# Kernel tuning notes

Hardware: AMD Instinct MI355X
Metric: run time of the kernel (lower is better)

## Reference

```python
import jax, jax.numpy as jnp
import numpy as np

SEQ = 784  # 28*28, hard-coded by the module's view() calls
RES_CH = 32
DILATIONS = [1, 2, 4, 8, 16] * 2  # layer_size=5, stack_size=2


def setup_inputs() -> dict:
    key = jax.random.key(0)
    ks = jax.random.split(key, 9)
    B = 2048
    s = 0.1
    return {
        "x": jax.random.normal(ks[0], (B, 1, 28, 28), dtype=jnp.float32),
        "w_causal": jax.random.normal(ks[1], (RES_CH, 1, 2), dtype=jnp.float32) * s,
        "b_causal": jax.random.normal(ks[2], (RES_CH,), dtype=jnp.float32) * s,
        "w_dil": jax.random.normal(ks[3], (10, 2 * RES_CH, RES_CH, 2), dtype=jnp.float32) * s,
        "b_dil": jax.random.normal(ks[4], (10, 2 * RES_CH), dtype=jnp.float32) * s,
        "w_res": jax.random.normal(ks[5], (10, RES_CH, RES_CH), dtype=jnp.float32) * s,
        "b_res": jax.random.normal(ks[6], (10, RES_CH), dtype=jnp.float32) * s,
        "w_out": jax.random.normal(ks[7], (1, RES_CH), dtype=jnp.float32) * s,
        "b_out": jax.random.normal(ks[8], (1,), dtype=jnp.float32) * s,
    }


def _shift_right(h, d):
    # causal left-pad by d, keep original length: out[:, :, t] = h[:, :, t - d]
    return jnp.pad(h, ((0, 0), (0, 0), (d, 0)))[:, :, :SEQ]


def reference(x, w_causal, b_causal, w_dil, b_dil, w_res, b_res, w_out, b_out):
    B = x.shape[0]
    h = x.reshape(B, 1, SEQ)
    # Mask-A causal conv (kernel=2, dilation=1, pad [2,0], drop last):
    # y[t] = W[:,:,0] @ x[t-2] + W[:,:,1] @ x[t-1]  (strictly causal)
    y = (
        jnp.einsum("oi,bit->bot", w_causal[:, :, 0], _shift_right(h, 2))
        + jnp.einsum("oi,bit->bot", w_causal[:, :, 1], _shift_right(h, 1))
        + b_causal[None, :, None]
    )
    h = y
    # Residual stack: Mask-B dilated conv -> gated tanh*sigmoid -> 1x1 conv -> residual add
    for i, d in enumerate(DILATIONS):
        z = (
            jnp.einsum("oi,bit->bot", w_dil[i, :, :, 0], _shift_right(h, d))
            + jnp.einsum("oi,bit->bot", w_dil[i, :, :, 1], h)
            + b_dil[i][None, :, None]
        )  # [B, 2*RES_CH, SEQ]
        o1, o2 = z[:, :RES_CH], z[:, RES_CH:]
        gated = jnp.tanh(o1) * jax.nn.sigmoid(o2)
        h = h + jnp.einsum("oi,bit->bot", w_res[i], gated) + b_res[i][None, :, None]
    logits = jnp.einsum("oi,bit->bot", w_out, h) + b_out[None, :, None]
    return logits.reshape(B, 1, 28, 28)
```

## Files before the change

### kernel.cpp

```cpp
#include <hip/hip_runtime.h>

#define SEQ   784
#define PADT  16
#define NROW  (PADT + 784)
#define NWAVE 8
#define BLK   (NWAVE * 64)
#define LDS_BYTES (NROW * 32 * 2)

#define WS_WR_OFF 81920
#define WS_BD_OFF 102400
#define SC_TANH (-2.885390082f)
#define SC_SIGM (-1.442695041f)

typedef __attribute__((ext_vector_type(8))) short  short8;
typedef __attribute__((ext_vector_type(4))) float  float4v;
typedef __attribute__((ext_vector_type(2))) unsigned int uint2v;

#if __has_builtin(__builtin_amdgcn_cvt_pk_bf16_f32)
typedef __attribute__((ext_vector_type(2))) __bf16 bf16x2;
__device__ __forceinline__ unsigned int pk_rne(float lo, float hi) {
    union { bf16x2 v; unsigned int u; } r;
    r.v = __builtin_amdgcn_cvt_pk_bf16_f32(lo, hi);
    return r.u;
}
#else
__device__ __forceinline__ unsigned int pk_rne(float lo, float hi) {
    unsigned int a = __float_as_uint(lo);
    unsigned int b = __float_as_uint(hi);
    a += 0x7fffu + ((a >> 16) & 1u);
    b += 0x7fffu + ((b >> 16) & 1u);
    return __builtin_amdgcn_perm(b, a, 0x07060302);
}
#endif
__device__ __forceinline__ unsigned short f2bf(float f) {
    unsigned int a = __float_as_uint(f);
    a += 0x7fffu + ((a >> 16) & 1u);
    return (unsigned short)(a >> 16);
}
__device__ __forceinline__ void gate_pair(float a1, float b1, float a2, float b2,
                                          float& g1, float& g2) {
    a1 = __builtin_amdgcn_fmed3f(a1, -30.f, 30.f);
    b1 = __builtin_amdgcn_fmed3f(b1, -30.f, 30.f);
    a2 = __builtin_amdgcn_fmed3f(a2, -30.f, 30.f);
    b2 = __builtin_amdgcn_fmed3f(b2, -30.f, 30.f);
    float ta1 = __builtin_amdgcn_exp2f(a1), tb1 = __builtin_amdgcn_exp2f(b1);
    float ta2 = __builtin_amdgcn_exp2f(a2), tb2 = __builtin_amdgcn_exp2f(b2);
    float p1 = (1.0f + ta1) * (1.0f + tb1);
    float p2 = (1.0f + ta2) * (1.0f + tb2);
    float r  = __builtin_amdgcn_rcpf(p1 * p2);
    g1 = (1.0f - ta1) * p2 * r;
    g2 = (1.0f - ta2) * p1 * r;
}

__global__ void __launch_bounds__(64) prep_kernel(
    const float* __restrict__ w_dil, const float* __restrict__ b_dil,
    const float* __restrict__ w_res, unsigned char* __restrict__ ws)
{
    const int L    = blockIdx.x;
    const int lane = threadIdx.x;
    const int m    = lane & 15;
    const int q    = lane >> 4;
    short8* WSA = (short8*)ws;
    short8* WSR = (short8*)(ws + WS_WR_OFF);
    float*  WSB = (float*)(ws + WS_BD_OFF);

    #pragma unroll
    for (int rt = 0; rt < 4; ++rt) {
        const float sc = (rt < 2) ? SC_TANH : SC_SIGM;
        const float4* wp = (const float4*)(w_dil + (((L * 64 + rt * 16 + m) * 32) + q * 8) * 2);
        float4 c0 = wp[0], c1 = wp[1], c2 = wp[2], c3 = wp[3];
        union { unsigned int i[4]; short8 v; } u0, u1;
        u0.i[0] = pk_rne(sc * c0.x, sc * c0.z); u0.i[1] = pk_rne(sc * c1.x, sc * c1.z);
        u0.i[2] = pk_rne(sc * c2.x, sc * c2.z); u0.i[3] = pk_rne(sc * c3.x, sc * c3.z);
        u1.i[0] = pk_rne(sc * c0.y, sc * c0.w); u1.i[1] = pk_rne(sc * c1.y, sc * c1.w);
        u1.i[2] = pk_rne(sc * c2.y, sc * c2.w); u1.i[3] = pk_rne(sc * c3.y, sc * c3.w);
        WSA[((L * 4 + rt) * 2 + 0) * 64 + lane] = u0.v;
        WSA[((L * 4 + rt) * 2 + 1) * 64 + lane] = u1.v;
    }
    #pragma unroll
    for (int rt = 0; rt < 2; ++rt) {
        const float4* wp = (const float4*)(w_res + (L * 32 + rt * 16 + m) * 32 + q * 8);
        float4 d0 = wp[0], d1 = wp[1];
        union { unsigned int i[4]; short8 v; } u;
        u.i[0] = pk_rne(d0.x, d0.y); u.i[1] = pk_rne(d0.z, d0.w);
        u.i[2] = pk_rne(d1.x, d1.y); u.i[3] = pk_rne(d1.z, d1.w);
        WSR[(L * 2 + rt) * 64 + lane] = u.v;
    }
    WSB[L * 64 + lane] = b_dil[L * 64 + lane] * ((lane < 32) ? SC_TANH : SC_SIGM);
}

__global__ void __launch_bounds__(BLK, 4) wavenet_kernel(
    const float* __restrict__ x,
    const float* __restrict__ w_causal,
    const float* __restrict__ b_causal,
    const float* __restrict__ b_res,
    const float* __restrict__ w_out,
    const float* __restrict__ b_out,
    const unsigned char* __restrict__ ws,
    float* __restrict__ out)
{
    extern __shared__ unsigned short lds[];
    unsigned short* H = lds;

    const int tid = threadIdx.x;
    const int b   = blockIdx.x;

    {
        unsigned int* p = (unsigned int*)H;
        if (tid < PADT * 16) p[tid] = 0u;
    }

    {
        int o = tid & 31;
        const int gsh = (o >> 3) << 3;
        const int oo  = o & 7;
        float wc0 = w_causal[o * 2 + 0];
        float wc1 = w_causal[o * 2 + 1];
        float bc  = b_causal[o];
        const float* xb = x + b * SEQ;
        for (int idx = tid; idx < SEQ * 32; idx += BLK) {
            int t = idx >> 5;
            float v = bc;
            if (t >= 2) v += wc0 * xb[t - 2];
            if (t >= 1) v += wc1 * xb[t - 1];
            int r = PADT + t;
            int sw = ((r >> 1) & 3) << 3;
            H[r * 32 + (gsh ^ sw) + oo] = f2bf(v);
        }
    }
    __syncthreads();

    const int lane = tid & 63;
    const int wave = tid >> 6;
    const int m    = lane & 15;
    const int q    = lane >> 4;
    const int adr1 = (32 * (q & 1) + m) * 4;
    const int adr2 = adr1 + 64;
    const int hi   = q >> 1;
    const int rowu0 = PADT + wave * 16 + m;
    const int su    = (rowu0 >> 1) & 3;
    const int offBu = ((q ^ su) << 3);
    const int offH1 = (((q >> 1) ^ su) << 3) + 4 * (q & 1);
    const int offH2 = ((((q >> 1) + 2) ^ su) << 3) + 4 * (q & 1);

    short8 I0, I1;
    #pragma unroll
    for (int j = 0; j < 8; ++j) {
        I0[j] = (q * 8 + j == m)      ? (short)0x3F80 : (short)0;
        I1[j] = (q * 8 + j == m + 16) ? (short)0x3F80 : (short)0;
    }

    const short8* WSA = (const short8*)ws;
    const short8* WSR = (const short8*)(ws + WS_WR_OFF);
    const float*  WSB = (const float*)(ws + WS_BD_OFF);

    const int dil[10] = {1, 2, 4, 8, 16, 1, 2, 4, 8, 16};

    for (int L = 0; L < 10; ++L) {
        const int d = dil[L];

        short8 WA[4][2], WR[2];
        #pragma unroll
        for (int rt = 0; rt < 4; ++rt) {
            WA[rt][0] = WSA[((L * 4 + rt) * 2 + 0) * 64 + lane];
            WA[rt][1] = WSA[((L * 4 + rt) * 2 + 1) * 64 + lane];
        }
        WR[0] = WSR[(L * 2 + 0) * 64 + lane];
        WR[1] = WSR[(L * 2 + 1) * 64 + lane];
        float4v BDv[4], BRv[2];
        #pragma unroll
        for (int rt = 0; rt < 4; ++rt)
            BDv[rt] = *(const float4v*)(WSB + L * 64 + rt * 16 + q * 4);
        #pragma unroll
        for (int rt = 0; rt < 2; ++rt) {
            const float* bp = b_res + L * 32 + rt * 16 + q * 4;
            BRv[rt] = (float4v){bp[0], bp[1], bp[2], bp[3]};
        }
        const int rs0   = rowu0 - d;
        const int offBs = ((q ^ ((rs0 >> 1) & 3)) << 3);

        auto do_tile = [&](int s, uint2v& n0, uint2v& n1) {
            const int rbase  = (rowu0 + s * (NWAVE * 16)) * 32;
            const int rbases = (rs0   + s * (NWAVE * 16)) * 32;
            const short8 Bs = *(const short8*)(H + rbases + offBs);
            const short8 Bu = *(const short8*)(H + rbase + offBu);

            float4v r0 = BRv[0], r1 = BRv[1];
            r0 = __builtin_amdgcn_mfma_f32_16x16x32_bf16(I0, Bu, r0, 0, 0, 0);
            r1 = __builtin_amdgcn_mfma_f32_16x16x32_bf16(I1, Bu, r1, 0, 0, 0);

            float4v a0 = BDv[0], a1 = BDv[1], a2 = BDv[2], a3 = BDv[3];
            a0 = __builtin_amdgcn_mfma_f32_16x16x32_bf16(WA[0][0], Bs, a0, 0, 0, 0);
            a0 = __builtin_amdgcn_mfma_f32_16x16x32_bf16(WA[0][1], Bu, a0, 0, 0, 0);
            a1 = __builtin_amdgcn_mfma_f32_16x16x32_bf16(WA[1][0], Bs, a1, 0, 0, 0);
            a1 = __builtin_amdgcn_mfma_f32_16x16x32_bf16(WA[1][1], Bu, a1, 0, 0, 0);
            a2 = __builtin_amdgcn_mfma_f32_16x16x32_bf16(WA[2][0], Bs, a2, 0, 0, 0);
            a2 = __builtin_amdgcn_mfma_f32_16x16x32_bf16(WA[2][1], Bu, a2, 0, 0, 0);
            a3 = __builtin_amdgcn_mfma_f32_16x16x32_bf16(WA[3][0], Bs, a3, 0, 0, 0);
            a3 = __builtin_amdgcn_mfma_f32_16x16x32_bf16(WA[3][1], Bu, a3, 0, 0, 0);

            float g00, g01, g02, g03, g10, g11, g12, g13;
            gate_pair(a0[0], a2[0], a0[1], a2[1], g00, g01);
            gate_pair(a0[2], a2[2], a0[3], a2[3], g02, g03);
            gate_pair(a1[0], a3[0], a1[1], a3[1], g10, g11);
            gate_pair(a1[2], a3[2], a1[3], a3[3], g12, g13);
            int P0 = (int)pk_rne(g00, g01), P1 = (int)pk_rne(g02, g03);
            int P2 = (int)pk_rne(g10, g11), P3 = (int)pk_rne(g12, g13);

            int A0 = __builtin_amdgcn_ds_bpermute(adr1, P0);
            int A1 = __builtin_amdgcn_ds_bpermute(adr1, P1);
            int A2 = __builtin_amdgcn_ds_bpermute(adr1, P2);
            int A3 = __builtin_amdgcn_ds_bpermute(adr1, P3);
            int C0 = __builtin_amdgcn_ds_bpermute(adr2, P0);
            int C1 = __builtin_amdgcn_ds_bpermute(adr2, P1);
            int C2 = __builtin_amdgcn_ds_bpermute(adr2, P2);
            int C3 = __builtin_amdgcn_ds_bpermute(adr2, P3);
            union { int i[4]; short8 v; } ug;
            ug.i[0] = hi ? A2 : A0; ug.i[1] = hi ? A3 : A1;
            ug.i[2] = hi ? C2 : C0; ug.i[3] = hi ? C3 : C1;
            const short8 Gf = ug.v;

            r0 = __builtin_amdgcn_mfma_f32_16x16x32_bf16(WR[0], Gf, r0, 0, 0, 0);
            r1 = __builtin_amdgcn_mfma_f32_16x16x32_bf16(WR[1], Gf, r1, 0, 0, 0);

            n0 = (uint2v){pk_rne(r0[0], r0[1]), pk_rne(r0[2], r0[3])};
            n1 = (uint2v){pk_rne(r1[0], r1[1]), pk_rne(r1[2], r1[3])};
        };
        auto store_tile = [&](int s, const uint2v& n0, const uint2v& n1) {
            const int rbase = (rowu0 + s * (NWAVE * 16)) * 32;
            *(uint2v*)(H + rbase + offH1) = n0;
            *(uint2v*)(H + rbase + offH2) = n1;
        };

        uint2v A0v[4], A1v[4], B0v[3], B1v[3];
        do_tile(3, A0v[0], A1v[0]);
        do_tile(4, A0v[1], A1v[1]);
        do_tile(5, A0v[2], A1v[2]);
        if (wave == 0) do_tile(6, A0v[3], A1v[3]);
        __syncthreads();
        store_tile(3, A0v[0], A1v[0]);
        store_tile(4, A0v[1], A1v[1]);
        store_tile(5, A0v[2], A1v[2]);
        if (wave == 0) store_tile(6, A0v[3], A1v[3]);
        do_tile(0, B0v[0], B1v[0]);
        do_tile(1, B0v[1], B1v[1]);
        do_tile(2, B0v[2], B1v[2]);
        __syncthreads();
        store_tile(0, B0v[0], B1v[0]);
        store_tile(1, B0v[1], B1v[1]);
        store_tile(2, B0v[2], B1v[2]);
        __syncthreads();
    }

    {
        float wo[32];
        #pragma unroll
        for (int k = 0; k < 32; ++k) wo[k] = w_out[k];
        float bo = b_out[0];
        for (int t = tid; t < SEQ; t += BLK) {
            int r = PADT + t;
            int sw = ((r >> 1) & 3) << 3;
            const unsigned short* hp = H + r * 32;
            float s = bo;
            #pragma unroll
            for (int kk = 0; kk < 32; kk += 4) {
                int c = ((((kk >> 3) << 3) ^ sw)) + (kk & 7);
                uint2v hh = *(const uint2v*)(hp + c);
                s += wo[kk]     * __uint_as_float(hh.x << 16);
                s += wo[kk + 1] * __uint_as_float(hh.x & 0xffff0000u);
                s += wo[kk + 2] * __uint_as_float(hh.y << 16);
                s += wo[kk + 3] * __uint_as_float(hh.y & 0xffff0000u);
            }
            out[b * SEQ + t] = s;
        }
    }
}

extern "C" void kernel_launch(void* const* d_in, const int* in_sizes, int n_in,
                              void* d_out, int out_size, void* d_ws, size_t ws_size,
                              hipStream_t stream) {
    const float* x        = (const float*)d_in[0];
    const float* w_causal = (const float*)d_in[1];
    const float* b_causal = (const float*)d_in[2];
    const float* w_dil    = (const float*)d_in[3];
    const float* b_dil    = (const float*)d_in[4];
    const float* w_res    = (const float*)d_in[5];
    const float* b_res    = (const float*)d_in[6];
    const float* w_out    = (const float*)d_in[7];
    const float* b_out    = (const float*)d_in[8];
    float* out = (float*)d_out;
    unsigned char* ws = (unsigned char*)d_ws;

    const int B = in_sizes[0] / SEQ;

    prep_kernel<<<10, 64, 0, stream>>>(w_dil, b_dil, w_res, ws);
    wavenet_kernel<<<B, BLK, LDS_BYTES, stream>>>(
        x, w_causal, b_causal, b_res, w_out, b_out, ws, out);
}
```

Before: 481.4 us.

## Split each sequence across two blocks with overlapping receptive-field halo

Each batch element is now processed by two blocks: one covers timesteps 0-399, the other recomputes from 336 (a 64-step halo matching the receptive field of 62) through 783 and outputs only 400-783. LDS per block roughly halves and the grid doubles, which is meant to raise occupancy and shorten per-block critical paths. The cost is about 14% redundant compute in the halo region and duplicated causal-conv setup.

Result: slower. 552.0 us (+14.7%).

```diff
diff --git a/kernel.cpp b/kernel.cpp
--- a/kernel.cpp
+++ b/kernel.cpp
@@ -2,10 +2,10 @@
 
 #define SEQ   784
 #define PADT  16
-#define NROW  (PADT + 784)
 #define NWAVE 8
 #define BLK   (NWAVE * 64)
-#define LDS_BYTES (NROW * 32 * 2)
+#define NROWB (PADT + 448)
+#define LDS_BYTES (NROWB * 32 * 2)
 
 #define WS_WR_OFF 81920
 #define WS_BD_OFF 102400
@@ -102,8 +102,15 @@
     extern __shared__ unsigned short lds[];
     unsigned short* H = lds;
 
-    const int tid = threadIdx.x;
-    const int b   = blockIdx.x;
+    const int tid  = threadIdx.x;
+    const int bid  = blockIdx.x;
+    const int b    = bid >> 1;
+    const int part = bid & 1;
+    const int t0     = part ? 336 : 0;
+    const int nrow   = part ? (PADT + 448) : (PADT + 400);
+    const int ntt    = part ? 28 : 25;
+    const int out_lo = part ? 400 : 0;
+    const int n_out  = part ? 384 : 400;
 
     {
         unsigned int* p = (unsigned int*)H;
@@ -118,12 +125,13 @@
         float wc1 = w_causal[o * 2 + 1];
         float bc  = b_causal[o];
         const float* xb = x + b * SEQ;
-        for (int idx = tid; idx < SEQ * 32; idx += BLK) {
-            int t = idx >> 5;
+        const int span = nrow - PADT;
+        for (int idx = tid; idx < span * 32; idx += BLK) {
+            int t = t0 + (idx >> 5);
             float v = bc;
             if (t >= 2) v += wc0 * xb[t - 2];
             if (t >= 1) v += wc1 * xb[t - 1];
-            int r = PADT + t;
+            int r = PADT + (idx >> 5);
             int sw = ((r >> 1) & 3) << 3;
             H[r * 32 + (gsh ^ sw) + oo] = f2bf(v);
         }
@@ -142,6 +150,7 @@
     const int offBu = ((q ^ su) << 3);
     const int offH1 = (((q >> 1) ^ su) << 3) + 4 * (q & 1);
     const int offH2 = ((((q >> 1) + 2) ^ su) << 3) + 4 * (q & 1);
+    const bool act3 = (wave + 24) < ntt;
 
     short8 I0, I1;
     #pragma unroll
@@ -232,23 +241,17 @@
             *(uint2v*)(H + rbase + offH2) = n1;
         };
 
-        uint2v A0v[4], A1v[4], B0v[3], B1v[3];
-        do_tile(3, A0v[0], A1v[0]);
-        do_tile(4, A0v[1], A1v[1]);
-        do_tile(5, A0v[2], A1v[2]);
-        if (wave == 0) do_tile(6, A0v[3], A1v[3]);
+        uint2v A0v[2], A1v[2], B0v[2], B1v[2];
+        do_tile(2, A0v[0], A1v[0]);
+        if (act3) do_tile(3, A0v[1], A1v[1]);
         __syncthreads();
-        store_tile(3, A0v[0], A1v[0]);
-        store_tile(4, A0v[1], A1v[1]);
-        store_tile(5, A0v[2], A1v[2]);
-        if (wave == 0) store_tile(6, A0v[3], A1v[3]);
+        store_tile(2, A0v[0], A1v[0]);
+        if (act3) store_tile(3, A0v[1], A1v[1]);
         do_tile(0, B0v[0], B1v[0]);
         do_tile(1, B0v[1], B1v[1]);
-        do_tile(2, B0v[2], B1v[2]);
         __syncthreads();
         store_tile(0, B0v[0], B1v[0]);
         store_tile(1, B0v[1], B1v[1]);
-        store_tile(2, B0v[2], B1v[2]);
         __syncthreads();
     }
 
@@ -257,8 +260,9 @@
         #pragma unroll
         for (int k = 0; k < 32; ++k) wo[k] = w_out[k];
         float bo = b_out[0];
-        for (int t = tid; t < SEQ; t += BLK) {
-            int r = PADT + t;
+        for (int i = tid; i < n_out; i += BLK) {
+            int t = out_lo + i;
+            int r = PADT + t - t0;
             int sw = ((r >> 1) & 3) << 3;
             const unsigned short* hp = H + r * 32;
             float s = bo;
@@ -294,6 +298,6 @@
     const int B = in_sizes[0] / SEQ;
 
     prep_kernel<<<10, 64, 0, stream>>>(w_dil, b_dil, w_res, ws);
-    wavenet_kernel<<<B, BLK, LDS_BYTES, stream>>>(
+    wavenet_kernel<<<B * 2, BLK, LDS_BYTES, stream>>>(
         x, w_causal, b_causal, b_res, w_out, b_out, ws, out);
 }
```
